# Kernel tuning notes

Measured on AMD Instinct MI355X. Metric: run time of the kernel, lower is better.

The kernel has to match this reference:

```python
import jax, jax.numpy as jnp
from jax import lax
import numpy as np

VOCAB, IN_DIM, MEM_DIM, SEQ = 100000, 256, 512, 2048
PAD = 0


def setup_inputs() -> dict:
    key = jax.random.key(0)
    k = jax.random.split(key, 7)
    emb = jax.random.normal(k[0], (VOCAB, IN_DIM), dtype=jnp.float32)
    emb = emb.at[PAD].set(0.0)  # padding_idx row is zero
    s_ih = 1.0 / np.sqrt(IN_DIM)
    s_hh = 1.0 / np.sqrt(MEM_DIM)
    return {
        "linputs": jax.random.randint(k[1], (SEQ,), 0, VOCAB, dtype=jnp.int64),
        "rinputs": jax.random.randint(k[2], (SEQ,), 0, VOCAB, dtype=jnp.int64),
        "emb": emb,
        "W_ih": jax.random.normal(k[3], (4 * MEM_DIM, IN_DIM), dtype=jnp.float32) * s_ih,
        "W_hh": jax.random.normal(k[4], (4 * MEM_DIM, MEM_DIM), dtype=jnp.float32) * s_hh,
        "b_ih": jax.random.normal(k[5], (4 * MEM_DIM,), dtype=jnp.float32) * s_hh,
        "b_hh": jax.random.normal(k[6], (4 * MEM_DIM,), dtype=jnp.float32) * s_hh,
    }


def _lstm_last_h(x_seq, W_ih, W_hh, b):
    # x_seq: [S, in_dim]. Returns h_T [mem_dim]. PyTorch gate order: i, f, g, o.
    H = W_hh.shape[1]
    # precompute input projections for all timesteps (one big GEMM)
    xp = x_seq @ W_ih.T + b  # [S, 4H]
    def step(carry, xg):
        h, c = carry
        gates = xg + h @ W_hh.T  # [4H]
        i = jax.nn.sigmoid(gates[:H])
        f = jax.nn.sigmoid(gates[H:2 * H])
        g = jnp.tanh(gates[2 * H:3 * H])
        o = jax.nn.sigmoid(gates[3 * H:])
        c = f * c + i * g
        h = o * jnp.tanh(c)
        return (h, c), None
    init = (jnp.zeros((H,), x_seq.dtype), jnp.zeros((H,), x_seq.dtype))
    (h, _), _ = lax.scan(step, init, xp)
    return h


def reference(linputs, rinputs, emb, W_ih, W_hh, b_ih, b_hh):
    b = b_ih + b_hh
    lx = emb[linputs]  # [S, in_dim]
    rx = emb[rinputs]
    lh = _lstm_last_h(lx, W_ih, W_hh, b)
    rh = _lstm_last_h(rx, W_ih, W_hh, b)
    return jnp.exp(-jnp.sum(jnp.abs(lh - rh)))
```

## Files before the change

### kernel.cpp

```cpp
#include <hip/hip_runtime.h>
#include <hip/hip_bf16.h>

#define SEQL  2048
#define IND   256
#define MEMD  512
#define G4    2048
#define NWG   16
#define VOCABN 100000

#define MB_SEQ   (NWG * 2 * MEMD)
#define MB_CONS  (2 * MEMD)

typedef __attribute__((ext_vector_type(4))) unsigned uintx4;
typedef __attribute__((ext_vector_type(2))) _Float16 half2v;

__device__ __forceinline__ unsigned short f2h_bits(float f) {
  _Float16 h = (_Float16)f;
  return __builtin_bit_cast(unsigned short, h);
}
__device__ __forceinline__ float h2f(unsigned bits) {
  return (float)__builtin_bit_cast(_Float16, (unsigned short)(bits & 0xffffu));
}

template <int CTRL>
__device__ __forceinline__ float dpp_fold_add(float v) {
  int x = __builtin_amdgcn_update_dpp(0, __float_as_int(v), CTRL, 0xf, 0xf, true);
  return v + __int_as_float(x);
}

__global__ void init_k(unsigned* __restrict__ mb) {
  int i = blockIdx.x * blockDim.x + threadIdx.x;
  if (i < 2 * MB_SEQ) mb[i] = 0u;
}

__global__ __launch_bounds__(256) void xp_gemm(
    const int* __restrict__ lin, const int* __restrict__ rin,
    const float* __restrict__ emb, const float* __restrict__ W_ih,
    const float* __restrict__ b_ih, const float* __restrict__ b_hh,
    unsigned short* __restrict__ xp) {
  __shared__ float As[64][68];
  __shared__ float Bs[64][68];
  const int s = blockIdx.z;
  const int* ids = (s == 0) ? lin : rin;
  const int t0 = blockIdx.x * 64;
  const int n0 = blockIdx.y * 64;
  const int tid = threadIdx.x;
  const int tx = tid & 15, ty = tid >> 4;

  float acc[4][4];
#pragma unroll
  for (int i = 0; i < 4; ++i)
#pragma unroll
    for (int j = 0; j < 4; ++j) acc[i][j] = 0.f;

  for (int kc = 0; kc < IND; kc += 64) {
#pragma unroll
    for (int j = 0; j < 4; ++j) {
      int fi  = tid + 256 * j;
      int row = fi >> 4;
      int c4  = fi & 15;
      int id  = ids[t0 + row];
      id = max(0, min(id, VOCABN - 1));
      const float4 va = *(const float4*)(emb + (size_t)id * IND + kc + c4 * 4);
      As[c4 * 4 + 0][row] = va.x; As[c4 * 4 + 1][row] = va.y;
      As[c4 * 4 + 2][row] = va.z; As[c4 * 4 + 3][row] = va.w;
      const float4 vb = *(const float4*)(W_ih + (size_t)(n0 + row) * IND + kc + c4 * 4);
      Bs[c4 * 4 + 0][row] = vb.x; Bs[c4 * 4 + 1][row] = vb.y;
      Bs[c4 * 4 + 2][row] = vb.z; Bs[c4 * 4 + 3][row] = vb.w;
    }
    __syncthreads();
#pragma unroll 8
    for (int k = 0; k < 64; ++k) {
      const float4 a = *(const float4*)&As[k][tx * 4];
      const float4 b = *(const float4*)&Bs[k][ty * 4];
      acc[0][0] = fmaf(a.x, b.x, acc[0][0]); acc[0][1] = fmaf(a.x, b.y, acc[0][1]);
      acc[0][2] = fmaf(a.x, b.z, acc[0][2]); acc[0][3] = fmaf(a.x, b.w, acc[0][3]);
      acc[1][0] = fmaf(a.y, b.x, acc[1][0]); acc[1][1] = fmaf(a.y, b.y, acc[1][1]);
      acc[1][2] = fmaf(a.y, b.z, acc[1][2]); acc[1][3] = fmaf(a.y, b.w, acc[1][3]);
      acc[2][0] = fmaf(a.z, b.x, acc[2][0]); acc[2][1] = fmaf(a.z, b.y, acc[2][1]);
      acc[2][2] = fmaf(a.z, b.z, acc[2][2]); acc[2][3] = fmaf(a.z, b.w, acc[2][3]);
      acc[3][0] = fmaf(a.w, b.x, acc[3][0]); acc[3][1] = fmaf(a.w, b.y, acc[3][1]);
      acc[3][2] = fmaf(a.w, b.z, acc[3][2]); acc[3][3] = fmaf(a.w, b.w, acc[3][3]);
    }
    __syncthreads();
  }
#pragma unroll
  for (int ri = 0; ri < 4; ++ri) {
#pragma unroll
    for (int bj = 0; bj < 4; ++bj) {
      int t = t0 + tx * 4 + ri;
      int n = n0 + ty * 4 + bj;
      float v = acc[ri][bj] + b_ih[n] + b_hh[n];
      int w = (n & 511) >> 5;
      int gate = n >> 9;
      int hd = n & 31;
      int pos = w * 128 + hd * 4 + gate;
      xp[((size_t)s * SEQL + t) * G4 + pos] = f2h_bits(v);
    }
  }
}

__global__ __launch_bounds__(512, 2) void lstm_rec(
    const float* __restrict__ W_hh,
    const unsigned short* __restrict__ xp,
    unsigned* __restrict__ mb) {
  __shared__ unsigned hlds[16 * 20];
  const int blk = blockIdx.x;
  const int s = blk & 1;
  const int w = blk >> 1;
  const int tid = threadIdx.x;
  const int lane = tid & 63;
  const int wv = tid >> 6;
  const int cg = tid & 15;
  const int rg = tid >> 4;

  half2v wreg[4][16];
#pragma unroll
  for (int g = 0; g < 4; ++g) {
    const float* src = W_hh + ((size_t)g * MEMD + w * 32 + rg) * MEMD + cg * 32;
#pragma unroll
    for (int q = 0; q < 8; ++q) {
      const float4 v = *(const float4*)(src + q * 4);
      half2v p0; p0.x = (_Float16)v.x; p0.y = (_Float16)v.y;
      half2v p1; p1.x = (_Float16)v.z; p1.y = (_Float16)v.w;
      wreg[g][q * 2 + 0] = p0;
      wreg[g][q * 2 + 1] = p1;
    }
  }

  unsigned* mbs = mb + s * MB_SEQ;
  unsigned* mymb = mbs + w * MB_CONS;
  const unsigned short* xq0 = xp + (size_t)s * SEQL * G4 + w * 128 + rg * 4;
  float cst = 0.f;

  ushort4 xg_cur = *(const ushort4*)xq0;

  for (int t = 0; t < SEQL; ++t) {
    ushort4 xg_next;
    {
      int tn = (t + 1 < SEQL) ? t + 1 : t;
      xg_next = *(const ushort4*)(xq0 + (size_t)tn * G4);
    }

    if (wv == 0) {
      const unsigned* hr = mymb + (t & 1) * MEMD + 8 * lane;
      unsigned long long a0 = (unsigned long long)hr;
      unsigned long long a1 = (unsigned long long)(hr + 4);
      uintx4 va, vb;
      const unsigned want = (unsigned)t;
      int guard = 0;
      for (;;) {
        asm volatile(
            "global_load_dwordx4 %0, %2, off sc0 sc1\n\t"
            "global_load_dwordx4 %1, %3, off sc0 sc1\n\t"
            "s_waitcnt vmcnt(0)"
            : "=&v"(va), "=&v"(vb)
            : "v"(a0), "v"(a1)
            : "memory");
        bool good = (va.x >> 16) == want && (va.y >> 16) == want &&
                    (va.z >> 16) == want && (va.w >> 16) == want &&
                    (vb.x >> 16) == want && (vb.y >> 16) == want &&
                    (vb.z >> 16) == want && (vb.w >> 16) == want;
        if (__all(good)) break;
        if (++guard > (1 << 16)) break;
      }
      uintx4 pk;
      pk.x = (va.x & 0xffffu) | (va.y << 16);
      pk.y = (va.z & 0xffffu) | (va.w << 16);
      pk.z = (vb.x & 0xffffu) | (vb.y << 16);
      pk.w = (vb.z & 0xffffu) | (vb.w << 16);
      *(uintx4*)&hlds[(lane >> 2) * 20 + (lane & 3) * 4] = pk;
    }
    __syncthreads();

    half2v hp[16];
    {
      const uintx4* hq = (const uintx4*)&hlds[cg * 20];
#pragma unroll
      for (int q = 0; q < 4; ++q) {
        uintx4 u = hq[q];
        hp[q * 4 + 0] = __builtin_bit_cast(half2v, u.x);
        hp[q * 4 + 1] = __builtin_bit_cast(half2v, u.y);
        hp[q * 4 + 2] = __builtin_bit_cast(half2v, u.z);
        hp[q * 4 + 3] = __builtin_bit_cast(half2v, u.w);
      }
    }
    float part[4] = {0.f, 0.f, 0.f, 0.f};
#pragma unroll
    for (int p = 0; p < 16; ++p) {
#pragma unroll
      for (int g = 0; g < 4; ++g)
        part[g] = __builtin_amdgcn_fdot2(wreg[g][p], hp[p], part[g], false);
    }
#pragma unroll
    for (int g = 0; g < 4; ++g) {
      part[g] = dpp_fold_add<0xB1>(part[g]);
      part[g] = dpp_fold_add<0x4E>(part[g]);
      part[g] = dpp_fold_add<0x141>(part[g]);
      part[g] = dpp_fold_add<0x140>(part[g]);
    }

    float gi = part[0] + h2f(xg_cur.x);
    float gf = part[1] + h2f(xg_cur.y);
    float gg = part[2] + h2f(xg_cur.z);
    float go = part[3] + h2f(xg_cur.w);
    float i_ = 1.f / (1.f + __expf(-gi));
    float f_ = 1.f / (1.f + __expf(-gf));
    float ggc = fminf(fmaxf(gg, -15.f), 15.f);
    float e2 = __expf(-2.f * ggc);
    float g_ = (1.f - e2) / (1.f + e2);
    float o_ = 1.f / (1.f + __expf(-go));
    cst = f_ * cst + i_ * g_;
    float cc = fminf(fmaxf(cst, -15.f), 15.f);
    float e2c = __expf(-2.f * cc);
    float th = (1.f - e2c) / (1.f + e2c);
    float h_ = o_ * th;

    unsigned pw = (((unsigned)(t + 1)) << 16) | (unsigned)f2h_bits(h_);
    unsigned q1 = __shfl(pw, 16, 64);
    unsigned q2 = __shfl(pw, 32, 64);
    unsigned q3 = __shfl(pw, 48, 64);
    if (lane < 16) {
      uintx4 val;
      val.x = pw; val.y = q1; val.z = q2; val.w = q3;
      unsigned long long addr = (unsigned long long)(
          mbs + lane * MB_CONS + ((t + 1) & 1) * MEMD + w * 32 + wv * 4);
      asm volatile("global_store_dwordx4 %0, %1, off sc0 sc1"
                   :: "v"(addr), "v"(val) : "memory");
    }
    xg_cur = xg_next;
  }
}

__global__ __launch_bounds__(512) void finish_k(const unsigned* __restrict__ mb,
                                                float* __restrict__ out) {
  const int tid = threadIdx.x;
  float l = h2f(mb[tid]);
  float r = h2f(mb[MB_SEQ + tid]);
  float d = fabsf(l - r);
#pragma unroll
  for (int m = 32; m >= 1; m >>= 1) d += __shfl_xor(d, m, 64);
  __shared__ float wsum[8];
  if ((tid & 63) == 0) wsum[tid >> 6] = d;
  __syncthreads();
  if (tid == 0) {
    float sum = 0.f;
#pragma unroll
    for (int i = 0; i < 8; ++i) sum += wsum[i];
    out[0] = expf(-sum);
  }
}

extern "C" void kernel_launch(void* const* d_in, const int* in_sizes, int n_in,
                              void* d_out, int out_size, void* d_ws, size_t ws_size,
                              hipStream_t stream) {
  const int*   lin  = (const int*)d_in[0];
  const int*   rin  = (const int*)d_in[1];
  const float* emb  = (const float*)d_in[2];
  const float* W_ih = (const float*)d_in[3];
  const float* W_hh = (const float*)d_in[4];
  const float* b_ih = (const float*)d_in[5];
  const float* b_hh = (const float*)d_in[6];
  float* out = (float*)d_out;

  unsigned char* ws = (unsigned char*)d_ws;
  unsigned short* xp = (unsigned short*)ws;
  unsigned* mb = (unsigned*)(ws + (size_t)2 * SEQL * G4 * sizeof(unsigned short));

  hipLaunchKernelGGL(init_k, dim3(2 * MB_SEQ / 1024), dim3(1024), 0, stream, mb);
  hipLaunchKernelGGL(xp_gemm, dim3(SEQL / 64, G4 / 64, 2), dim3(256), 0, stream,
                     lin, rin, emb, W_ih, b_ih, b_hh, xp);
  hipLaunchKernelGGL(lstm_rec, dim3(2 * NWG), dim3(512), 0, stream, W_hh, xp, mb);
  hipLaunchKernelGGL(finish_k, dim3(1), dim3(512), 0, stream, mb, out);
}
```

Measured before the change: 3.590 ms.

## Process both LSTM sequences in the same workgroups, halving grid-wide mailbox sync

The recurrent kernel now runs 16 workgroups, each handling both the left and right sequences at once, instead of 32 workgroups each handling one sequence. Every workgroup keeps the same register-resident W_hh slice and reuses it for two dot products per step. The h exchange through global memory polls and publishes both sequences in a single mailbox round per step. The aim is to spread the per-step synchronisation latency over twice the useful work. In exchange each step does twice the arithmetic and gate math per thread, which adds register pressure and lengthens the serial step.

```diff
diff --git a/kernel.cpp b/kernel.cpp
--- a/kernel.cpp
+++ b/kernel.cpp
@@ -8,8 +8,8 @@
 #define NWG   16
 #define VOCABN 100000
 
-#define MB_SEQ   (NWG * 2 * MEMD)
-#define MB_CONS  (2 * MEMD)
+#define MB_CONS  (2 * 2 * MEMD)
+#define MB_TOT   (NWG * MB_CONS)
 
 typedef __attribute__((ext_vector_type(4))) unsigned uintx4;
 typedef __attribute__((ext_vector_type(2))) _Float16 half2v;
@@ -28,9 +28,23 @@
   return v + __int_as_float(x);
 }
 
+__device__ __forceinline__ float lstm_gate(float gi, float gf, float gg, float go,
+                                           float& c) {
+  float i_ = 1.f / (1.f + __expf(-gi));
+  float f_ = 1.f / (1.f + __expf(-gf));
+  float ggc = fminf(fmaxf(gg, -15.f), 15.f);
+  float e2 = __expf(-2.f * ggc);
+  float g_ = (1.f - e2) / (1.f + e2);
+  float o_ = 1.f / (1.f + __expf(-go));
+  c = f_ * c + i_ * g_;
+  float cc = fminf(fmaxf(c, -15.f), 15.f);
+  float e2c = __expf(-2.f * cc);
+  return o_ * (1.f - e2c) / (1.f + e2c);
+}
+
 __global__ void init_k(unsigned* __restrict__ mb) {
   int i = blockIdx.x * blockDim.x + threadIdx.x;
-  if (i < 2 * MB_SEQ) mb[i] = 0u;
+  if (i < MB_TOT) mb[i] = 0u;
 }
 
 __global__ __launch_bounds__(256) void xp_gemm(
@@ -104,10 +118,8 @@
     const float* __restrict__ W_hh,
     const unsigned short* __restrict__ xp,
     unsigned* __restrict__ mb) {
-  __shared__ unsigned hlds[16 * 20];
-  const int blk = blockIdx.x;
-  const int s = blk & 1;
-  const int w = blk >> 1;
+  __shared__ unsigned hlds[2][16 * 20];
+  const int w = blockIdx.x;
   const int tid = threadIdx.x;
   const int lane = tid & 63;
   const int wv = tid >> 6;
@@ -128,107 +140,127 @@
     }
   }
 
-  unsigned* mbs = mb + s * MB_SEQ;
-  unsigned* mymb = mbs + w * MB_CONS;
-  const unsigned short* xq0 = xp + (size_t)s * SEQL * G4 + w * 128 + rg * 4;
-  float cst = 0.f;
-
-  ushort4 xg_cur = *(const ushort4*)xq0;
+  unsigned* mymb = mb + w * MB_CONS;
+  const unsigned short* xqL = xp + w * 128 + rg * 4;
+  const unsigned short* xqR = xqL + (size_t)SEQL * G4;
+  float cstL = 0.f, cstR = 0.f;
+
+  ushort4 xgL = *(const ushort4*)xqL;
+  ushort4 xgR = *(const ushort4*)xqR;
 
   for (int t = 0; t < SEQL; ++t) {
-    ushort4 xg_next;
+    ushort4 xgLn, xgRn;
     {
       int tn = (t + 1 < SEQL) ? t + 1 : t;
-      xg_next = *(const ushort4*)(xq0 + (size_t)tn * G4);
+      xgLn = *(const ushort4*)(xqL + (size_t)tn * G4);
+      xgRn = *(const ushort4*)(xqR + (size_t)tn * G4);
     }
 
     if (wv == 0) {
-      const unsigned* hr = mymb + (t & 1) * MEMD + 8 * lane;
+      const unsigned* hr = mymb + (t & 1) * (2 * MEMD) + 8 * lane;
       unsigned long long a0 = (unsigned long long)hr;
-      unsigned long long a1 = (unsigned long long)(hr + 4);
-      uintx4 va, vb;
+      unsigned long long a1 = a0 + 16;
+      unsigned long long a2 = (unsigned long long)(hr + MEMD);
+      unsigned long long a3 = a2 + 16;
+      uintx4 va, vb, vc, vd;
       const unsigned want = (unsigned)t;
       int guard = 0;
       for (;;) {
         asm volatile(
-            "global_load_dwordx4 %0, %2, off sc0 sc1\n\t"
-            "global_load_dwordx4 %1, %3, off sc0 sc1\n\t"
+            "global_load_dwordx4 %0, %4, off sc0 sc1\n\t"
+            "global_load_dwordx4 %1, %5, off sc0 sc1\n\t"
+            "global_load_dwordx4 %2, %6, off sc0 sc1\n\t"
+            "global_load_dwordx4 %3, %7, off sc0 sc1\n\t"
             "s_waitcnt vmcnt(0)"
-            : "=&v"(va), "=&v"(vb)
-            : "v"(a0), "v"(a1)
+            : "=&v"(va), "=&v"(vb), "=&v"(vc), "=&v"(vd)
+            : "v"(a0), "v"(a1), "v"(a2), "v"(a3)
             : "memory");
         bool good = (va.x >> 16) == want && (va.y >> 16) == want &&
                     (va.z >> 16) == want && (va.w >> 16) == want &&
                     (vb.x >> 16) == want && (vb.y >> 16) == want &&
-                    (vb.z >> 16) == want && (vb.w >> 16) == want;
+                    (vb.z >> 16) == want && (vb.w >> 16) == want &&
+                    (vc.x >> 16) == want && (vc.y >> 16) == want &&
+                    (vc.z >> 16) == want && (vc.w >> 16) == want &&
+                    (vd.x >> 16) == want && (vd.y >> 16) == want &&
+                    (vd.z >> 16) == want && (vd.w >> 16) == want;
         if (__all(good)) break;
         if (++guard > (1 << 16)) break;
       }
+      int hoff = (lane >> 2) * 20 + (lane & 3) * 4;
       uintx4 pk;
       pk.x = (va.x & 0xffffu) | (va.y << 16);
       pk.y = (va.z & 0xffffu) | (va.w << 16);
       pk.z = (vb.x & 0xffffu) | (vb.y << 16);
       pk.w = (vb.z & 0xffffu) | (vb.w << 16);
-      *(uintx4*)&hlds[(lane >> 2) * 20 + (lane & 3) * 4] = pk;
+      *(uintx4*)&hlds[0][hoff] = pk;
+      pk.x = (vc.x & 0xffffu) | (vc.y << 16);
+      pk.y = (vc.z & 0xffffu) | (vc.w << 16);
+      pk.z = (vd.x & 0xffffu) | (vd.y << 16);
+      pk.w = (vd.z & 0xffffu) | (vd.w << 16);
+      *(uintx4*)&hlds[1][hoff] = pk;
     }
     __syncthreads();
 
-    half2v hp[16];
+    half2v hpL[16], hpR[16];
     {
-      const uintx4* hq = (const uintx4*)&hlds[cg * 20];
+      const uintx4* hqL = (const uintx4*)&hlds[0][cg * 20];
+      const uintx4* hqR = (const uintx4*)&hlds[1][cg * 20];
 #pragma unroll
       for (int q = 0; q < 4; ++q) {
-        uintx4 u = hq[q];
-        hp[q * 4 + 0] = __builtin_bit_cast(half2v, u.x);
-        hp[q * 4 + 1] = __builtin_bit_cast(half2v, u.y);
-        hp[q * 4 + 2] = __builtin_bit_cast(half2v, u.z);
-        hp[q * 4 + 3] = __builtin_bit_cast(half2v, u.w);
+        uintx4 u = hqL[q];
+        hpL[q * 4 + 0] = __builtin_bit_cast(half2v, u.x);
+        hpL[q * 4 + 1] = __builtin_bit_cast(half2v, u.y);
+        hpL[q * 4 + 2] = __builtin_bit_cast(half2v, u.z);
+        hpL[q * 4 + 3] = __builtin_bit_cast(half2v, u.w);
+        uintx4 v2 = hqR[q];
+        hpR[q * 4 + 0] = __builtin_bit_cast(half2v, v2.x);
+        hpR[q * 4 + 1] = __builtin_bit_cast(half2v, v2.y);
+        hpR[q * 4 + 2] = __builtin_bit_cast(half2v, v2.z);
+        hpR[q * 4 + 3] = __builtin_bit_cast(half2v, v2.w);
       }
     }
-    float part[4] = {0.f, 0.f, 0.f, 0.f};
+    float pL[4] = {0.f, 0.f, 0.f, 0.f};
+    float pR[4] = {0.f, 0.f, 0.f, 0.f};
 #pragma unroll
     for (int p = 0; p < 16; ++p) {
 #pragma unroll
-      for (int g = 0; g < 4; ++g)
-        part[g] = __builtin_amdgcn_fdot2(wreg[g][p], hp[p], part[g], false);
+      for (int g = 0; g < 4; ++g) {
+        pL[g] = __builtin_amdgcn_fdot2(wreg[g][p], hpL[p], pL[g], false);
+        pR[g] = __builtin_amdgcn_fdot2(wreg[g][p], hpR[p], pR[g], false);
+      }
     }
 #pragma unroll
     for (int g = 0; g < 4; ++g) {
-      part[g] = dpp_fold_add<0xB1>(part[g]);
-      part[g] = dpp_fold_add<0x4E>(part[g]);
-      part[g] = dpp_fold_add<0x141>(part[g]);
-      part[g] = dpp_fold_add<0x140>(part[g]);
-    }
-
-    float gi = part[0] + h2f(xg_cur.x);
-    float gf = part[1] + h2f(xg_cur.y);
-    float gg = part[2] + h2f(xg_cur.z);
-    float go = part[3] + h2f(xg_cur.w);
-    float i_ = 1.f / (1.f + __expf(-gi));
-    float f_ = 1.f / (1.f + __expf(-gf));
-    float ggc = fminf(fmaxf(gg, -15.f), 15.f);
-    float e2 = __expf(-2.f * ggc);
-    float g_ = (1.f - e2) / (1.f + e2);
-    float o_ = 1.f / (1.f + __expf(-go));
-    cst = f_ * cst + i_ * g_;
-    float cc = fminf(fmaxf(cst, -15.f), 15.f);
-    float e2c = __expf(-2.f * cc);
-    float th = (1.f - e2c) / (1.f + e2c);
-    float h_ = o_ * th;
-
-    unsigned pw = (((unsigned)(t + 1)) << 16) | (unsigned)f2h_bits(h_);
-    unsigned q1 = __shfl(pw, 16, 64);
-    unsigned q2 = __shfl(pw, 32, 64);
-    unsigned q3 = __shfl(pw, 48, 64);
-    if (lane < 16) {
-      uintx4 val;
-      val.x = pw; val.y = q1; val.z = q2; val.w = q3;
+      pL[g] = dpp_fold_add<0xB1>(pL[g]);  pR[g] = dpp_fold_add<0xB1>(pR[g]);
+      pL[g] = dpp_fold_add<0x4E>(pL[g]);  pR[g] = dpp_fold_add<0x4E>(pR[g]);
+      pL[g] = dpp_fold_add<0x141>(pL[g]); pR[g] = dpp_fold_add<0x141>(pR[g]);
+      pL[g] = dpp_fold_add<0x140>(pL[g]); pR[g] = dpp_fold_add<0x140>(pR[g]);
+    }
+
+    float hL = lstm_gate(pL[0] + h2f(xgL.x), pL[1] + h2f(xgL.y),
+                         pL[2] + h2f(xgL.z), pL[3] + h2f(xgL.w), cstL);
+    float hR = lstm_gate(pR[0] + h2f(xgR.x), pR[1] + h2f(xgR.y),
+                         pR[2] + h2f(xgR.z), pR[3] + h2f(xgR.w), cstR);
+
+    unsigned ep = ((unsigned)(t + 1)) << 16;
+    unsigned pwL = ep | (unsigned)f2h_bits(hL);
+    unsigned pwR = ep | (unsigned)f2h_bits(hR);
+    uintx4 valL, valR;
+    valL.x = pwL; valL.y = __shfl(pwL, 16, 64);
+    valL.z = __shfl(pwL, 32, 64); valL.w = __shfl(pwL, 48, 64);
+    valR.x = pwR; valR.y = __shfl(pwR, 16, 64);
+    valR.z = __shfl(pwR, 32, 64); valR.w = __shfl(pwR, 48, 64);
+    if (lane < 32) {
+      uintx4 val = (lane < 16) ? valL : valR;
+      unsigned cons = lane & 15;
+      unsigned seqsel = lane >> 4;
       unsigned long long addr = (unsigned long long)(
-          mbs + lane * MB_CONS + ((t + 1) & 1) * MEMD + w * 32 + wv * 4);
+          mb + cons * MB_CONS + ((t + 1) & 1) * (2 * MEMD) + seqsel * MEMD +
+          w * 32 + wv * 4);
       asm volatile("global_store_dwordx4 %0, %1, off sc0 sc1"
                    :: "v"(addr), "v"(val) : "memory");
     }
-    xg_cur = xg_next;
+    xgL = xgLn; xgR = xgRn;
   }
 }
 
@@ -236,7 +268,7 @@
                                                 float* __restrict__ out) {
   const int tid = threadIdx.x;
   float l = h2f(mb[tid]);
-  float r = h2f(mb[MB_SEQ + tid]);
+  float r = h2f(mb[MEMD + tid]);
   float d = fabsf(l - r);
 #pragma unroll
   for (int m = 32; m >= 1; m >>= 1) d += __shfl_xor(d, m, 64);
@@ -267,9 +299,9 @@
   unsigned short* xp = (unsigned short*)ws;
   unsigned* mb = (unsigned*)(ws + (size_t)2 * SEQL * G4 * sizeof(unsigned short));
 
-  hipLaunchKernelGGL(init_k, dim3(2 * MB_SEQ / 1024), dim3(1024), 0, stream, mb);
+  hipLaunchKernelGGL(init_k, dim3(MB_TOT / 1024), dim3(1024), 0, stream, mb);
   hipLaunchKernelGGL(xp_gemm, dim3(SEQL / 64, G4 / 64, 2), dim3(256), 0, stream,
                      lin, rin, emb, W_ih, b_ih, b_hh, xp);
-  hipLaunchKernelGGL(lstm_rec, dim3(2 * NWG), dim3(512), 0, stream, W_hh, xp, mb);
+  hipLaunchKernelGGL(lstm_rec, dim3(NWG), dim3(512), 0, stream, W_hh, xp, mb);
   hipLaunchKernelGGL(finish_k, dim3(1), dim3(512), 0, stream, mb, out);
 }
```

Result: slower. 5.740 ms (+59.9%).
